# Optimization experiments

Hardware: AMD Instinct MI355X
Metric: run time of the kernel (lower is better)

## Reference

```python
import jax, jax.numpy as jnp
import numpy as np

N = 30000       # nodes
E = 480000      # edges (before self loops)
IN = 128        # in_channels
H1, C1 = 5, 64  # conv1 heads, per-head channels
OUT = 64        # out_channels (conv2, heads=1)
PE = 100000     # pos/neg edges for decode
NEG_SLOPE = 0.2


def setup_inputs() -> dict:
    key = jax.random.key(0)
    ks = jax.random.split(key, 12)
    return {
        "x": jax.random.normal(ks[0], (N, IN), dtype=jnp.float32),
        "edge_index": jax.random.randint(ks[1], (2, E), 0, N),
        "pos_edge_index": jax.random.randint(ks[2], (2, PE), 0, N),
        "neg_edge_index": jax.random.randint(ks[3], (2, PE), 0, N),
        "W1": jax.random.normal(ks[4], (IN, H1 * C1), dtype=jnp.float32) * 0.05,
        "att_src1": jax.random.normal(ks[5], (H1, C1), dtype=jnp.float32) * 0.1,
        "att_dst1": jax.random.normal(ks[6], (H1, C1), dtype=jnp.float32) * 0.1,
        "b1": jnp.zeros((H1 * C1,), dtype=jnp.float32),
        "W2": jax.random.normal(ks[7], (H1 * C1, OUT), dtype=jnp.float32) * 0.05,
        "att_src2": jax.random.normal(ks[8], (1, OUT), dtype=jnp.float32) * 0.1,
        "att_dst2": jax.random.normal(ks[9], (1, OUT), dtype=jnp.float32) * 0.1,
        "b2": jnp.zeros((OUT,), dtype=jnp.float32),
    }


def gat_conv(x, edge_index, W, att_src, att_dst, bias, heads, out_ch):
    """PyG GATConv: add self loops, linear proj, edge softmax, scatter-sum, concat heads."""
    n = x.shape[0]
    loops = jnp.arange(n)
    src = jnp.concatenate([edge_index[0], loops])  # message sources j
    dst = jnp.concatenate([edge_index[1], loops])  # message targets i
    h = (x @ W).reshape(n, heads, out_ch)          # [N,H,C]
    a_src = jnp.sum(h * att_src, axis=-1)          # [N,H]
    a_dst = jnp.sum(h * att_dst, axis=-1)          # [N,H]
    e = jax.nn.leaky_relu(a_src[src] + a_dst[dst], NEG_SLOPE)  # [E',H]
    # numerically-stable segment softmax over incoming edges of each dst node
    m = jax.ops.segment_max(e, dst, num_segments=n)
    m = jax.lax.stop_gradient(jnp.where(jnp.isfinite(m), m, 0.0))
    ex = jnp.exp(e - m[dst])
    s = jax.ops.segment_sum(ex, dst, num_segments=n)
    alpha = ex / (s[dst] + 1e-16)                  # [E',H]
    out = jax.ops.segment_sum(alpha[:, :, None] * h[src], dst, num_segments=n)  # [N,H,C]
    return out.reshape(n, heads * out_ch) + bias


def reference(x, edge_index, pos_edge_index, neg_edge_index,
              W1, att_src1, att_dst1, b1, W2, att_src2, att_dst2, b2):
    z = gat_conv(x, edge_index, W1, att_src1, att_dst1, b1, H1, C1)
    z = jax.nn.relu(z)
    z = gat_conv(z, edge_index, W2, att_src2, att_dst2, b2, 1, OUT)
    ei = jnp.concatenate([pos_edge_index, neg_edge_index], axis=-1)
    return jnp.sum(z[ei[0]] * z[ei[1]], axis=-1)  # [2*PE]
```

## Files before the change

### kernel.cpp

```cpp
#include <hip/hip_runtime.h>
#include <hip/hip_fp16.h>
#include <cstdint>
#include <cstddef>
#include <type_traits>

#define N_NODES 30000
#define N_EDGES 480000
#define N_EDGES_SL (N_EDGES + N_NODES)
#define IN_CH 128
#define HEADS1 5
#define C1 64
#define D1 (HEADS1 * C1)
#define OUT_CH 64
#define PE_CNT 100000
#define NEG_SLOPE 0.2f
#define BCAP 64
#define CPAD 32
#define GEMM1_BLOCKS 469
#define BUCKET_BLOCKS 128

typedef _Float16 f16x8 __attribute__((ext_vector_type(8)));
typedef _Float16 f16x2 __attribute__((ext_vector_type(2)));
typedef float fx4 __attribute__((ext_vector_type(4)));

#if defined(__has_builtin)
#if __has_builtin(__builtin_amdgcn_fdot2)
#define HAS_FDOT2 1
#endif
#endif

static __device__ __forceinline__ float leaky(float x) {
    return fmaxf(x, NEG_SLOPE * x);
}

template<int NH, int SP, typename AT>
static __device__ __forceinline__ void gemm_phase(const AT* __restrict__ A,
                                                  const __half* __restrict__ Wt,
                                                  __half* __restrict__ C, int K,
                                                  const float* __restrict__ att_src,
                                                  const float* __restrict__ att_dst,
                                                  float* __restrict__ as_out,
                                                  float* __restrict__ ad_out,
                                                  int slot, int nsl, int lane) {
    const int N = NH * 64;
    int q = lane >> 4, l16 = lane & 15;
    for (int tile = slot; tile < N_NODES / 16; tile += nsl) {
        int rowBase = tile * 16;
        int arow = rowBase + l16;
        fx4 zero4 = {0.f, 0.f, 0.f, 0.f};
        fx4 acc[NH][4];
#pragma unroll
        for (int h = 0; h < NH; ++h)
#pragma unroll
            for (int c = 0; c < 4; ++c) acc[h][c] = zero4;
        for (int kk = 0; kk < K; kk += 32) {
            f16x8 af;
            if constexpr (std::is_same<AT, float>::value) {
                const float4* s = (const float4*)(A + (size_t)arow * K + kk + q * 8);
                float4 v0 = s[0], v1 = s[1];
                af[0] = (_Float16)v0.x; af[1] = (_Float16)v0.y;
                af[2] = (_Float16)v0.z; af[3] = (_Float16)v0.w;
                af[4] = (_Float16)v1.x; af[5] = (_Float16)v1.y;
                af[6] = (_Float16)v1.z; af[7] = (_Float16)v1.w;
            } else {
                af = *(const f16x8*)((const __half*)A + (size_t)arow * K + kk + q * 8);
            }
#pragma unroll
            for (int h = 0; h < NH; ++h) {
#pragma unroll
                for (int c = 0; c < 4; ++c) {
                    int col = h * 64 + c * 16 + l16;
                    f16x8 bf = *(const f16x8*)(Wt + (size_t)col * K + kk + q * 8);
                    acc[h][c] = __builtin_amdgcn_mfma_f32_16x16x32_f16(af, bf, acc[h][c], 0, 0, 0);
                }
            }
        }
#pragma unroll
        for (int h = 0; h < NH; ++h) {
            float ps[4] = {0.f, 0.f, 0.f, 0.f};
            float pd[4] = {0.f, 0.f, 0.f, 0.f};
#pragma unroll
            for (int c = 0; c < 4; ++c) {
                int gcol = h * 64 + c * 16 + l16;
                float av = att_src[gcol];
                float dv = att_dst[gcol];
#pragma unroll
                for (int reg = 0; reg < 4; ++reg) {
                    int grow = rowBase + q * 4 + reg;
                    float val = acc[h][c][reg];
                    C[(size_t)grow * N + gcol] = __float2half(val);
                    ps[reg] += val * av;
                    pd[reg] += val * dv;
                }
            }
#pragma unroll
            for (int off = 1; off < 16; off <<= 1) {
#pragma unroll
                for (int reg = 0; reg < 4; ++reg) {
                    ps[reg] += __shfl_xor(ps[reg], off, 64);
                    pd[reg] += __shfl_xor(pd[reg], off, 64);
                }
            }
            if (l16 == 0) {
#pragma unroll
                for (int reg = 0; reg < 4; ++reg) {
                    int grow = rowBase + q * 4 + reg;
                    as_out[(size_t)grow * SP + h] = ps[reg];
                    ad_out[(size_t)grow * SP + h] = pd[reg];
                }
            }
        }
    }
}

__global__ __launch_bounds__(256) void k_init(int* __restrict__ cnt,
                                              int* __restrict__ ovfc,
                                              int* __restrict__ esrc2,
                                              const float* __restrict__ W1,
                                              __half* __restrict__ Wt1,
                                              const float* __restrict__ W2,
                                              __half* __restrict__ Wt2) {
    int t = blockIdx.x * 256 + threadIdx.x;
    int nthr = gridDim.x * 256;
    for (int i = t; i < N_NODES; i += nthr) {
        cnt[(size_t)i * CPAD] = 1;
        esrc2[i * BCAP] = i;
    }
    if (t == 0) *ovfc = 0;
    const int T1 = IN_CH * D1, T2 = D1 * OUT_CH;
    for (int idx = t; idx < T1 + T2; idx += nthr) {
        if (idx < T1) {
            int k = idx / D1, n = idx - k * D1;
            Wt1[(size_t)n * IN_CH + k] = __float2half(W1[idx]);
        } else {
            int i2 = idx - T1;
            int k = i2 / OUT_CH, n = i2 - k * OUT_CH;
            Wt2[(size_t)n * D1 + k] = __float2half(W2[i2]);
        }
    }
}

__global__ __launch_bounds__(256) void k_build_gemm1(const int* __restrict__ edge,
                                                     int* __restrict__ cnt,
                                                     int* __restrict__ esrc2,
                                                     int* __restrict__ ovf_cnt,
                                                     int* __restrict__ ovf,
                                                     const float* __restrict__ x,
                                                     const __half* __restrict__ Wt1,
                                                     __half* __restrict__ h1,
                                                     const float* __restrict__ att_src1,
                                                     const float* __restrict__ att_dst1,
                                                     float* __restrict__ as1,
                                                     float* __restrict__ ad1) {
    int lane = threadIdx.x & 63, wv = threadIdx.x >> 6;
    if (blockIdx.x < GEMM1_BLOCKS) {
        gemm_phase<HEADS1, 8, float>(x, Wt1, h1, IN_CH, att_src1, att_dst1, as1, ad1,
                                     blockIdx.x * 4 + wv, GEMM1_BLOCKS * 4, lane);
    } else {
        int t = (blockIdx.x - GEMM1_BLOCKS) * 256 + threadIdx.x;
        const int nthr = BUCKET_BLOCKS * 256;
        int e = t;
        for (; e + 3 * nthr < N_EDGES; e += 4 * nthr) {
            int e1 = e + nthr, e2 = e + 2 * nthr, e3 = e + 3 * nthr;
            int s0 = edge[e];  int d0 = edge[N_EDGES + e];
            int s1 = edge[e1]; int d1 = edge[N_EDGES + e1];
            int s2 = edge[e2]; int d2 = edge[N_EDGES + e2];
            int s3 = edge[e3]; int d3 = edge[N_EDGES + e3];
            int r0 = atomicAdd(&cnt[(size_t)d0 * CPAD], 1);
            int r1 = atomicAdd(&cnt[(size_t)d1 * CPAD], 1);
            int r2 = atomicAdd(&cnt[(size_t)d2 * CPAD], 1);
            int r3 = atomicAdd(&cnt[(size_t)d3 * CPAD], 1);
            if (r0 < BCAP) esrc2[d0 * BCAP + r0] = s0;
            else { int oi = atomicAdd(ovf_cnt, 1); ovf[2 * oi] = d0; ovf[2 * oi + 1] = s0; }
            if (r1 < BCAP) esrc2[d1 * BCAP + r1] = s1;
            else { int oi = atomicAdd(ovf_cnt, 1); ovf[2 * oi] = d1; ovf[2 * oi + 1] = s1; }
            if (r2 < BCAP) esrc2[d2 * BCAP + r2] = s2;
            else { int oi = atomicAdd(ovf_cnt, 1); ovf[2 * oi] = d2; ovf[2 * oi + 1] = s2; }
            if (r3 < BCAP) esrc2[d3 * BCAP + r3] = s3;
            else { int oi = atomicAdd(ovf_cnt, 1); ovf[2 * oi] = d3; ovf[2 * oi + 1] = s3; }
        }
        for (; e < N_EDGES; e += nthr) {
            int s = edge[e];
            int d = edge[N_EDGES + e];
            int r = atomicAdd(&cnt[(size_t)d * CPAD], 1);
            if (r < BCAP) {
                esrc2[d * BCAP + r] = s;
            } else {
                int oi = atomicAdd(ovf_cnt, 1);
                ovf[2 * oi] = d;
                ovf[2 * oi + 1] = s;
            }
        }
    }
}

template<int NH, bool RELU>
__global__ __launch_bounds__(256) void k_attn_agg(const int* __restrict__ cnt,
                                                  const int* __restrict__ esrc2,
                                                  const int* __restrict__ ovf_cnt,
                                                  const int* __restrict__ ovf,
                                                  const __half* __restrict__ hf,
                                                  const float* __restrict__ a_src,
                                                  const float* __restrict__ a_dst,
                                                  const float* __restrict__ bias,
                                                  __half* __restrict__ zout) {
    const int SP = (NH == 1) ? 1 : 8;
    __shared__ unsigned wpk[4][NH][64];
    __shared__ int jbuf[4][64];
    __shared__ float red[4][584];
    int node = (blockIdx.x * 256 + threadIdx.x) >> 6;
    int lane = threadIdx.x & 63;
    int wv = threadIdx.x >> 6;
    if (node >= N_NODES) return;
    int deg = cnt[(size_t)node * CPAD];
    const int RS = NH * 64;
    float da[NH];
    if constexpr (NH == 1) {
        da[0] = a_dst[node];
    } else {
        float4 d0 = *(const float4*)(a_dst + (size_t)node * SP);
        da[0] = d0.x; da[1] = d0.y; da[2] = d0.z; da[3] = d0.w;
        da[4] = a_dst[(size_t)node * SP + 4];
    }
    if (deg <= BCAP) {
        int es = lane >> 3, cg = lane & 7;
        int joff = 0;
        float e[NH];
#pragma unroll
        for (int h = 0; h < NH; ++h) e[h] = 0.f;
        if (lane < deg) {
            int j = esrc2[node * BCAP + lane];
            joff = j * RS;
            if constexpr (NH == 1) {
                e[0] = __expf(leaky(a_src[j] + da[0]));
            } else {
                float4 s0 = *(const float4*)(a_src + (size_t)j * SP);
                float s4 = a_src[(size_t)j * SP + 4];
                e[0] = __expf(leaky(s0.x + da[0]));
                e[1] = __expf(leaky(s0.y + da[1]));
                e[2] = __expf(leaky(s0.z + da[2]));
                e[3] = __expf(leaky(s0.w + da[3]));
                e[4] = __expf(leaky(s4 + da[4]));
            }
        }
        float s[NH];
#pragma unroll
        for (int h = 0; h < NH; ++h) s[h] = e[h];
#pragma unroll
        for (int off = 1; off < 64; off <<= 1) {
#pragma unroll
            for (int h = 0; h < NH; ++h) s[h] += __shfl_xor(s[h], off, 64);
        }
#pragma unroll
        for (int h = 0; h < NH; ++h) {
            float r = 1.f / (s[h] + 1e-16f);
            __half2 wn = __float2half2_rn(e[h] * r);
            wpk[wv][h][lane] = *(unsigned*)&wn;
        }
        jbuf[wv][lane] = joff;
#pragma unroll
        for (int h = 0; h < NH; ++h) {
            const __half* hbase = hf + h * 64 + cg * 8;
            __half2 acch[4] = {__half2{0, 0}, __half2{0, 0}, __half2{0, 0}, __half2{0, 0}};
            for (int k0 = 0; k0 < deg; k0 += 32) {
                int kA = k0 + es, kB = kA + 8, kC = kA + 16, kD = kA + 24;
                unsigned uA = wpk[wv][h][kA];
                unsigned uB = wpk[wv][h][kB];
                unsigned uC = wpk[wv][h][kC];
                unsigned uD = wpk[wv][h][kD];
                int jA = jbuf[wv][kA];
                int jB = jbuf[wv][kB];
                int jC = jbuf[wv][kC];
                int jD = jbuf[wv][kD];
                float4 vA = *(const float4*)(hbase + jA);
                float4 vB = *(const float4*)(hbase + jB);
                float4 vC = *(const float4*)(hbase + jC);
                float4 vD = *(const float4*)(hbase + jD);
                __half2 hwA = *(__half2*)&uA, hwB = *(__half2*)&uB;
                __half2 hwC = *(__half2*)&uC, hwD = *(__half2*)&uD;
                const __half2* pA = (const __half2*)&vA;
                const __half2* pB = (const __half2*)&vB;
                const __half2* pC = (const __half2*)&vC;
                const __half2* pD = (const __half2*)&vD;
#pragma unroll
                for (int i = 0; i < 4; ++i) {
                    acch[i] = __hfma2(pA[i], hwA, acch[i]);
                    acch[i] = __hfma2(pB[i], hwB, acch[i]);
                    acch[i] = __hfma2(pC[i], hwC, acch[i]);
                    acch[i] = __hfma2(pD[i], hwD, acch[i]);
                }
            }
#pragma unroll
            for (int i = 0; i < 4; ++i) {
                float2 f = __half22float2(acch[i]);
                red[wv][(cg * 8 + 2 * i) * 9 + es] = f.x;
                red[wv][(cg * 8 + 2 * i + 1) * 9 + es] = f.y;
            }
            float tot = 0.f;
#pragma unroll
            for (int e2 = 0; e2 < 8; ++e2)
                tot += red[wv][lane * 9 + e2];
            float o = tot + bias[h * 64 + lane];
            if (RELU) o = fmaxf(o, 0.f);
            zout[(size_t)node * RS + h * 64 + lane] = __float2half(o);
        }
    } else {
        int ovn = *ovf_cnt;
#pragma unroll
        for (int h = 0; h < NH; ++h) {
            float adsth = da[h];
            float sden = __expf(leaky(a_src[(size_t)esrc2[node * BCAP + lane] * SP + h] + adsth));
#pragma unroll
            for (int off = 1; off < 64; off <<= 1)
                sden += __shfl_xor(sden, off, 64);
            float s2 = 0.f;
            for (int k = lane; k < ovn; k += 64)
                if (ovf[2 * k] == node)
                    s2 += __expf(leaky(a_src[(size_t)ovf[2 * k + 1] * SP + h] + adsth));
#pragma unroll
            for (int off = 1; off < 64; off <<= 1)
                s2 += __shfl_xor(s2, off, 64);
            float r = 1.f / (sden + s2 + 1e-16f);
            float a = 0.f;
            for (int k = 0; k < BCAP; ++k) {
                int j = esrc2[node * BCAP + k];
                float w = __expf(leaky(a_src[(size_t)j * SP + h] + adsth));
                a += w * __half2float(hf[(size_t)j * RS + h * 64 + lane]);
            }
            for (int k = 0; k < ovn; ++k) {
                if (ovf[2 * k] == node) {
                    int j = ovf[2 * k + 1];
                    float w = __expf(leaky(a_src[(size_t)j * SP + h] + adsth));
                    a += w * __half2float(hf[(size_t)j * RS + h * 64 + lane]);
                }
            }
            float o = a * r + bias[h * 64 + lane];
            if (RELU) o = fmaxf(o, 0.f);
            zout[(size_t)node * RS + h * 64 + lane] = __float2half(o);
        }
    }
}

__global__ __launch_bounds__(256) void k_gemm2(const __half* __restrict__ z1,
                                               const __half* __restrict__ Wt2,
                                               __half* __restrict__ h2,
                                               const float* __restrict__ att_src2,
                                               const float* __restrict__ att_dst2,
                                               float* __restrict__ as2,
                                               float* __restrict__ ad2) {
    int lane = threadIdx.x & 63, wv = threadIdx.x >> 6;
    gemm_phase<1, 1, __half>(z1, Wt2, h2, D1, att_src2, att_dst2, as2, ad2,
                             blockIdx.x * 4 + wv, gridDim.x * 4, lane);
}

__global__ __launch_bounds__(256) void k_decode(const int* __restrict__ pos,
                                                const int* __restrict__ neg,
                                                const __half* __restrict__ z2,
                                                float* __restrict__ out) {
    int t = blockIdx.x * 256 + threadIdx.x;
    int e = t >> 3;
    int lc = t & 7;
    if (e >= 2 * PE_CNT) return;
    int a, b;
    if (e < PE_CNT) { a = pos[e]; b = pos[PE_CNT + e]; }
    else { int k = e - PE_CNT; a = neg[k]; b = neg[PE_CNT + k]; }
    union U { float4 f; f16x2 h[4]; __half2 hh[4]; } ua, ub;
    ua.f = *(const float4*)(z2 + (size_t)a * OUT_CH + lc * 8);
    ub.f = *(const float4*)(z2 + (size_t)b * OUT_CH + lc * 8);
    float v = 0.f;
#pragma unroll
    for (int i = 0; i < 4; ++i) {
#ifdef HAS_FDOT2
        v = __builtin_amdgcn_fdot2(ua.h[i], ub.h[i], v, false);
#else
        float2 fa = __half22float2(ua.hh[i]);
        float2 fb = __half22float2(ub.hh[i]);
        v += fa.x * fb.x + fa.y * fb.y;
#endif
    }
#pragma unroll
    for (int off = 1; off < 8; off <<= 1)
        v += __shfl_xor(v, off, 64);
    if (lc == 0) out[e] = v;
}

extern "C" void kernel_launch(void* const* d_in, const int* in_sizes, int n_in,
                              void* d_out, int out_size, void* d_ws, size_t ws_size,
                              hipStream_t stream) {
    const float* x        = (const float*)d_in[0];
    const int* edge_index = (const int*)d_in[1];
    const int* pos_ei     = (const int*)d_in[2];
    const int* neg_ei     = (const int*)d_in[3];
    const float* W1       = (const float*)d_in[4];
    const float* att_src1 = (const float*)d_in[5];
    const float* att_dst1 = (const float*)d_in[6];
    const float* b1       = (const float*)d_in[7];
    const float* W2       = (const float*)d_in[8];
    const float* att_src2 = (const float*)d_in[9];
    const float* att_dst2 = (const float*)d_in[10];
    const float* b2       = (const float*)d_in[11];
    float* out            = (float*)d_out;

    char* ws = (char*)d_ws;
    size_t off = 0;
    auto alloc = [&](size_t bytes) -> void* {
        void* p = ws + off;
        off = (off + bytes + 255) & ~(size_t)255;
        return p;
    };
    int* cnt     = (int*)alloc(sizeof(int) * (size_t)N_NODES * CPAD);
    int* ovfc    = (int*)alloc(sizeof(int) * 8);
    int* esrc2   = (int*)alloc(sizeof(int) * (size_t)N_NODES * BCAP);
    int* ovf     = (int*)alloc(sizeof(int) * (size_t)2 * N_EDGES_SL);
    __half* h1   = (__half*)alloc(sizeof(__half) * (size_t)N_NODES * D1);
    __half* z1   = (__half*)alloc(sizeof(__half) * (size_t)N_NODES * D1);
    __half* h2   = (__half*)alloc(sizeof(__half) * (size_t)N_NODES * OUT_CH);
    __half* z2   = (__half*)alloc(sizeof(__half) * (size_t)N_NODES * OUT_CH);
    __half* Wt1  = (__half*)alloc(sizeof(__half) * (size_t)D1 * IN_CH);
    __half* Wt2  = (__half*)alloc(sizeof(__half) * (size_t)OUT_CH * D1);
    float* as1   = (float*)alloc(sizeof(float) * (size_t)N_NODES * 8);
    float* ad1   = (float*)alloc(sizeof(float) * (size_t)N_NODES * 8);
    float* as2   = (float*)alloc(sizeof(float) * (size_t)N_NODES);
    float* ad2   = (float*)alloc(sizeof(float) * (size_t)N_NODES);

    k_init<<<240, 256, 0, stream>>>(cnt, ovfc, esrc2, W1, Wt1, W2, Wt2);
    k_build_gemm1<<<GEMM1_BLOCKS + BUCKET_BLOCKS, 256, 0, stream>>>(
        edge_index, cnt, esrc2, ovfc, ovf, x, Wt1, h1, att_src1, att_dst1, as1, ad1);
    k_attn_agg<HEADS1, true><<<(N_NODES + 3) / 4, 256, 0, stream>>>(
        cnt, esrc2, ovfc, ovf, h1, as1, ad1, b1, z1);
    k_gemm2<<<469, 256, 0, stream>>>(z1, Wt2, h2, att_src2, att_dst2, as2, ad2);
    k_attn_agg<1, false><<<(N_NODES + 3) / 4, 256, 0, stream>>>(
        cnt, esrc2, ovfc, ovf, h2, as2, ad2, b2, z2);
    k_decode<<<(2 * PE_CNT * 8 + 255) / 256, 256, 0, stream>>>(pos_ei, neg_ei, z2, out);

    (void)in_sizes; (void)n_in; (void)out_size; (void)ws_size;
}
```

Before: 208.3 us.

## Partition CSR bucketing by destination range with shared-memory counters

Replaces global-atomic edge bucketing with 32 blocks, each owning a contiguous range of destination nodes. Each block keeps its counters in LDS and writes final counts to a compact, unpadded cnt array. This removes contended global atomics and the padded counter array. In exchange every block must scan the whole edge list, adding redundant reads, and only 32 blocks do the bucketing, which may become the critical path next to the GEMM blocks.

```diff
diff --git a/kernel.cpp b/kernel.cpp
--- a/kernel.cpp
+++ b/kernel.cpp
@@ -15,9 +15,9 @@
 #define PE_CNT 100000
 #define NEG_SLOPE 0.2f
 #define BCAP 64
-#define CPAD 32
 #define GEMM1_BLOCKS 469
-#define BUCKET_BLOCKS 128
+#define PASS_BLOCKS 32
+#define NODES_PER_PB ((N_NODES + PASS_BLOCKS - 1) / PASS_BLOCKS)
 
 typedef _Float16 f16x8 __attribute__((ext_vector_type(8)));
 typedef _Float16 f16x2 __attribute__((ext_vector_type(2)));
@@ -113,8 +113,7 @@
     }
 }
 
-__global__ __launch_bounds__(256) void k_init(int* __restrict__ cnt,
-                                              int* __restrict__ ovfc,
+__global__ __launch_bounds__(256) void k_init(int* __restrict__ ovfc,
                                               int* __restrict__ esrc2,
                                               const float* __restrict__ W1,
                                               __half* __restrict__ Wt1,
@@ -122,10 +121,7 @@
                                               __half* __restrict__ Wt2) {
     int t = blockIdx.x * 256 + threadIdx.x;
     int nthr = gridDim.x * 256;
-    for (int i = t; i < N_NODES; i += nthr) {
-        cnt[(size_t)i * CPAD] = 1;
-        esrc2[i * BCAP] = i;
-    }
+    for (int i = t; i < N_NODES; i += nthr) esrc2[i * BCAP] = i;
     if (t == 0) *ovfc = 0;
     const int T1 = IN_CH * D1, T2 = D1 * OUT_CH;
     for (int idx = t; idx < T1 + T2; idx += nthr) {
@@ -152,45 +148,43 @@
                                                      const float* __restrict__ att_dst1,
                                                      float* __restrict__ as1,
                                                      float* __restrict__ ad1) {
+    __shared__ int lcnt[NODES_PER_PB];
     int lane = threadIdx.x & 63, wv = threadIdx.x >> 6;
     if (blockIdx.x < GEMM1_BLOCKS) {
         gemm_phase<HEADS1, 8, float>(x, Wt1, h1, IN_CH, att_src1, att_dst1, as1, ad1,
                                      blockIdx.x * 4 + wv, GEMM1_BLOCKS * 4, lane);
     } else {
-        int t = (blockIdx.x - GEMM1_BLOCKS) * 256 + threadIdx.x;
-        const int nthr = BUCKET_BLOCKS * 256;
-        int e = t;
-        for (; e + 3 * nthr < N_EDGES; e += 4 * nthr) {
-            int e1 = e + nthr, e2 = e + 2 * nthr, e3 = e + 3 * nthr;
-            int s0 = edge[e];  int d0 = edge[N_EDGES + e];
-            int s1 = edge[e1]; int d1 = edge[N_EDGES + e1];
-            int s2 = edge[e2]; int d2 = edge[N_EDGES + e2];
-            int s3 = edge[e3]; int d3 = edge[N_EDGES + e3];
-            int r0 = atomicAdd(&cnt[(size_t)d0 * CPAD], 1);
-            int r1 = atomicAdd(&cnt[(size_t)d1 * CPAD], 1);
-            int r2 = atomicAdd(&cnt[(size_t)d2 * CPAD], 1);
-            int r3 = atomicAdd(&cnt[(size_t)d3 * CPAD], 1);
-            if (r0 < BCAP) esrc2[d0 * BCAP + r0] = s0;
-            else { int oi = atomicAdd(ovf_cnt, 1); ovf[2 * oi] = d0; ovf[2 * oi + 1] = s0; }
-            if (r1 < BCAP) esrc2[d1 * BCAP + r1] = s1;
-            else { int oi = atomicAdd(ovf_cnt, 1); ovf[2 * oi] = d1; ovf[2 * oi + 1] = s1; }
-            if (r2 < BCAP) esrc2[d2 * BCAP + r2] = s2;
-            else { int oi = atomicAdd(ovf_cnt, 1); ovf[2 * oi] = d2; ovf[2 * oi + 1] = s2; }
-            if (r3 < BCAP) esrc2[d3 * BCAP + r3] = s3;
-            else { int oi = atomicAdd(ovf_cnt, 1); ovf[2 * oi] = d3; ovf[2 * oi + 1] = s3; }
-        }
-        for (; e < N_EDGES; e += nthr) {
-            int s = edge[e];
-            int d = edge[N_EDGES + e];
-            int r = atomicAdd(&cnt[(size_t)d * CPAD], 1);
-            if (r < BCAP) {
-                esrc2[d * BCAP + r] = s;
-            } else {
-                int oi = atomicAdd(ovf_cnt, 1);
-                ovf[2 * oi] = d;
-                ovf[2 * oi + 1] = s;
-            }
-        }
+        int pb = blockIdx.x - GEMM1_BLOCKS;
+        int lo = pb * NODES_PER_PB;
+        int hi = lo + NODES_PER_PB;
+        if (hi > N_NODES) hi = N_NODES;
+        int range = hi - lo;
+        for (int i = threadIdx.x; i < range; i += 256) lcnt[i] = 0;
+        __syncthreads();
+        for (int e = (threadIdx.x << 2); e < N_EDGES; e += 256 * 4) {
+            int4 dd = *(const int4*)(edge + N_EDGES + e);
+            int4 ss = *(const int4*)(edge + e);
+            int dv[4] = {dd.x, dd.y, dd.z, dd.w};
+            int sv[4] = {ss.x, ss.y, ss.z, ss.w};
+#pragma unroll
+            for (int u = 0; u < 4; ++u) {
+                int d = dv[u];
+                unsigned rel = (unsigned)(d - lo);
+                if (rel < (unsigned)range) {
+                    int rank = atomicAdd(&lcnt[rel], 1);
+                    if (rank < BCAP - 1) {
+                        esrc2[(d << 6) + 1 + rank] = sv[u];
+                    } else {
+                        int oi = atomicAdd(ovf_cnt, 1);
+                        ovf[2 * oi] = d;
+                        ovf[2 * oi + 1] = sv[u];
+                    }
+                }
+            }
+        }
+        __syncthreads();
+        for (int i = threadIdx.x; i < range; i += 256)
+            cnt[lo + i] = 1 + lcnt[i];
     }
 }
 
@@ -212,7 +206,7 @@
     int lane = threadIdx.x & 63;
     int wv = threadIdx.x >> 6;
     if (node >= N_NODES) return;
-    int deg = cnt[(size_t)node * CPAD];
+    int deg = cnt[node];
     const int RS = NH * 64;
     float da[NH];
     if constexpr (NH == 1) {
@@ -408,7 +402,7 @@
         off = (off + bytes + 255) & ~(size_t)255;
         return p;
     };
-    int* cnt     = (int*)alloc(sizeof(int) * (size_t)N_NODES * CPAD);
+    int* cnt     = (int*)alloc(sizeof(int) * N_NODES);
     int* ovfc    = (int*)alloc(sizeof(int) * 8);
     int* esrc2   = (int*)alloc(sizeof(int) * (size_t)N_NODES * BCAP);
     int* ovf     = (int*)alloc(sizeof(int) * (size_t)2 * N_EDGES_SL);
@@ -423,8 +417,8 @@
     float* as2   = (float*)alloc(sizeof(float) * (size_t)N_NODES);
     float* ad2   = (float*)alloc(sizeof(float) * (size_t)N_NODES);
 
-    k_init<<<240, 256, 0, stream>>>(cnt, ovfc, esrc2, W1, Wt1, W2, Wt2);
-    k_build_gemm1<<<GEMM1_BLOCKS + BUCKET_BLOCKS, 256, 0, stream>>>(
+    k_init<<<240, 256, 0, stream>>>(ovfc, esrc2, W1, Wt1, W2, Wt2);
+    k_build_gemm1<<<GEMM1_BLOCKS + PASS_BLOCKS, 256, 0, stream>>>(
         edge_index, cnt, esrc2, ovfc, ovf, x, Wt1, h1, att_src1, att_dst1, as1, ad1);
     k_attn_agg<HEADS1, true><<<(N_NODES + 3) / 4, 256, 0, stream>>>(
         cnt, esrc2, ovfc, ovf, h1, as1, ad1, b1, z1);
```

Measured after the change: 466.5 us. +123.9%, slower.
